# Kernel optimization log

Hardware: AMD Instinct MI355X
Metric: run time of the kernel (lower is better)

The kernel has to match this reference:

```python
import jax, jax.numpy as jnp
import numpy as np


def _square_distance(src, dst):
    # src: [B,N,C], dst: [B,M,C] -> [B,N,M] squared euclidean distances
    # ||s-d||^2 = -2 s.d + ||s||^2 + ||d||^2
    d = -2.0 * jnp.einsum('bnc,bmc->bnm', src, dst)
    d = d + jnp.sum(src * src, axis=-1)[:, :, None]
    d = d + jnp.sum(dst * dst, axis=-1)[:, None, :]
    return d


def setup_inputs() -> dict:
    key = jax.random.key(0)
    k1, k2 = jax.random.split(key)
    B, N, M, C = 8, 4096, 4096, 3
    f = jax.random.normal(k1, (B, N, C), dtype=jnp.float32)
    f_ = jax.random.normal(k2, (B, M, C), dtype=jnp.float32)
    return {"f": f, "f_": f_}


def reference(f, f_):
    dis = _square_distance(f, f_)          # [B,N,M]
    f2f_ = jnp.min(dis, axis=2)            # [B,N] nearest in f_ for each f point
    f_2f = jnp.min(dis, axis=1)            # [B,M] nearest in f for each f_ point
    d = jnp.mean(f2f_, axis=1) + jnp.mean(f_2f, axis=1)  # [B]
    return jnp.mean(d)
```

## Files before the change

### kernel.cpp

```cpp
#include <hip/hip_runtime.h>


typedef float v2f __attribute__((ext_vector_type(2)));

constexpr int B = 8;
constexpr int N = 4096;
constexpr int M = 4096;
constexpr int S = 16;
constexpr int TM = M / S;
constexpr int GPS = TM / 2;
constexpr int BLOCK = 256;
constexpr int Q = 8;
constexpr int QPB = BLOCK * Q;
constexpr int QCH = N / QPB;

__device__ __forceinline__ v2f pk_fma(v2f a, v2f b, v2f c) {
    v2f d;
    asm("v_pk_fma_f32 %0, %1, %2, %3" : "=v"(d) : "v"(a), "v"(b), "v"(c));
    return d;
}

__global__ __launch_bounds__(256, 2) void chamfer_dir_kernel(
    const float* __restrict__ f,
    const float* __restrict__ f_,
    unsigned int* __restrict__ minA,
    unsigned int* __restrict__ minB)
{
    __shared__ float4 sT[2 * GPS];

    const int dir = blockIdx.z;
    const int b   = blockIdx.y;
    const int seg = blockIdx.x & (S - 1);
    const int qc  = blockIdx.x >> 4;

    const float* qsrc = dir ? f_ : f;
    const float* tsrc = dir ? f  : f_;
    unsigned int* omin = dir ? minB : minA;

    {
        const int t = threadIdx.x;
        const float* tb = tsrc + ((size_t)b * M + (size_t)seg * TM + t) * 3;
        const float x = tb[0], y = tb[1], z = tb[2];
        const int g = t >> 1, h = t & 1;
        float* base = (float*)sT;
        base[8 * g + 0 + h] = -2.0f * x;
        base[8 * g + 2 + h] = -2.0f * y;
        base[8 * g + 4 + h] = -2.0f * z;
        base[8 * g + 6 + h] = x * x + y * y + z * z;
    }

    const int qbase = qc * QPB + threadIdx.x;
    const float* qb = qsrc + (size_t)b * N * 3;
    v2f qxv[Q], qyv[Q], qzv[Q];
    float qn[Q];
    #pragma unroll
    for (int j = 0; j < Q; ++j) {
        const int q = qbase + j * BLOCK;
        const float x = qb[3 * q + 0], y = qb[3 * q + 1], z = qb[3 * q + 2];
        qxv[j] = (v2f){x, x};
        qyv[j] = (v2f){y, y};
        qzv[j] = (v2f){z, z};
        qn[j] = x * x + y * y + z * z;
    }
    __syncthreads();

    float m[Q];
    #pragma unroll
    for (int j = 0; j < Q; ++j) m[j] = 3.402823466e+38f;

    #pragma unroll 2
    for (int g = 0; g < GPS; ++g) {
        const float4 r0 = sT[2 * g];
        const float4 r1 = sT[2 * g + 1];
        const v2f x01 = {r0.x, r0.y};
        const v2f y01 = {r0.z, r0.w};
        const v2f z01 = {r1.x, r1.y};
        const v2f w01 = {r1.z, r1.w};

        #pragma unroll
        for (int j = 0; j < Q; ++j) {
            v2f a = pk_fma(qzv[j], z01, w01);
            a = pk_fma(qyv[j], y01, a);
            a = pk_fma(qxv[j], x01, a);
            m[j] = fminf(fminf(m[j], a.x), a.y);
        }
    }

    #pragma unroll
    for (int j = 0; j < Q; ++j) {
        const float d = m[j] + qn[j];
        atomicMin(&omin[b * N + qbase + j * BLOCK], __float_as_uint(d));
    }
}

__global__ __launch_bounds__(256) void reduce_out_kernel(
    const uint4* __restrict__ mins,
    float* __restrict__ out)
{
    __shared__ float wsum[4];
    const int tid = threadIdx.x;
    const uint4 v = mins[blockIdx.x * 256 + tid];
    float s = (__uint_as_float(v.x) + __uint_as_float(v.y))
            + (__uint_as_float(v.z) + __uint_as_float(v.w));

    #pragma unroll
    for (int off = 32; off > 0; off >>= 1) s += __shfl_down(s, off, 64);
    if ((tid & 63) == 0) wsum[tid >> 6] = s;
    __syncthreads();
    if (tid == 0) {
        const float r = (wsum[0] + wsum[1]) + (wsum[2] + wsum[3]);
        atomicAdd(out, r * (1.0f / 32768.0f));
    }
}

extern "C" void kernel_launch(void* const* d_in, const int* in_sizes, int n_in,
                              void* d_out, int out_size, void* d_ws, size_t ws_size,
                              hipStream_t stream) {
    (void)in_sizes; (void)n_in; (void)out_size; (void)ws_size;
    const float* f  = (const float*)d_in[0];
    const float* f_ = (const float*)d_in[1];
    float* out = (float*)d_out;

    unsigned int* minA = (unsigned int*)d_ws;
    unsigned int* minB = minA + (size_t)B * N;

    dim3 grid(QCH * S, B, 2);
    chamfer_dir_kernel<<<grid, BLOCK, 0, stream>>>(f, f_, minA, minB);

    reduce_out_kernel<<<64, 256, 0, stream>>>((const uint4*)minA, out);
}
```

Measured before the change: 77.33 us.

## Compute both chamfer directions in one pass with split-bf16 MFMA tiles

```diff
diff --git a/kernel.cpp b/kernel.cpp
--- a/kernel.cpp
+++ b/kernel.cpp
@@ -1,96 +1,147 @@
 #include <hip/hip_runtime.h>
 
 
-typedef float v2f __attribute__((ext_vector_type(2)));
+typedef __attribute__((ext_vector_type(8))) short bf16x8;
+typedef __attribute__((ext_vector_type(4))) float f32x4;
 
 constexpr int B = 8;
 constexpr int N = 4096;
 constexpr int M = 4096;
-constexpr int S = 16;
-constexpr int TM = M / S;
-constexpr int GPS = TM / 2;
-constexpr int BLOCK = 256;
-constexpr int Q = 8;
-constexpr int QPB = BLOCK * Q;
-constexpr int QCH = N / QPB;
 
-__device__ __forceinline__ v2f pk_fma(v2f a, v2f b, v2f c) {
-    v2f d;
-    asm("v_pk_fma_f32 %0, %1, %2, %3" : "=v"(d) : "v"(a), "v"(b), "v"(c));
-    return d;
+constexpr int ROWS_PER_BLOCK = 128;
+constexpr int COL_CHUNK = 2048;
+constexpr int SEG = 512;
+constexpr int SEGS = COL_CHUNK / SEG;
+constexpr int CTILES = SEG / 16;
+
+static __device__ __forceinline__ unsigned short f2bf(float v) {
+    unsigned u = __float_as_uint(v);
+    return (unsigned short)((u + 0x7FFFu + ((u >> 16) & 1u)) >> 16);
+}
+static __device__ __forceinline__ float bf2f(unsigned short b) {
+    return __uint_as_float(((unsigned)b) << 16);
+}
+static __device__ __forceinline__ void split3(float v, unsigned short& a,
+                                              unsigned short& b, unsigned short& c) {
+    a = f2bf(v); float r = v - bf2f(a);
+    b = f2bf(r); r -= bf2f(b);
+    c = f2bf(r);
 }
 
-__global__ __launch_bounds__(256, 2) void chamfer_dir_kernel(
+__global__ __launch_bounds__(256, 2) void chamfer_mfma_kernel(
     const float* __restrict__ f,
     const float* __restrict__ f_,
     unsigned int* __restrict__ minA,
     unsigned int* __restrict__ minB)
 {
-    __shared__ float4 sT[2 * GPS];
+    __shared__ unsigned short Bv[SEG][32];
+    __shared__ unsigned int cmin[COL_CHUNK];
 
-    const int dir = blockIdx.z;
-    const int b   = blockIdx.y;
-    const int seg = blockIdx.x & (S - 1);
-    const int qc  = blockIdx.x >> 4;
+    const int tid  = threadIdx.x;
+    const int lane = tid & 63;
+    const int w    = tid >> 6;
+    const int r    = lane & 15;
+    const int kg   = lane >> 4;
 
-    const float* qsrc = dir ? f_ : f;
-    const float* tsrc = dir ? f  : f_;
-    unsigned int* omin = dir ? minB : minA;
+    const int b  = blockIdx.y;
+    const int rc = blockIdx.x >> 1;
+    const int cc = blockIdx.x & 1;
 
-    {
-        const int t = threadIdx.x;
-        const float* tb = tsrc + ((size_t)b * M + (size_t)seg * TM + t) * 3;
-        const float x = tb[0], y = tb[1], z = tb[2];
-        const int g = t >> 1, h = t & 1;
-        float* base = (float*)sT;
-        base[8 * g + 0 + h] = -2.0f * x;
-        base[8 * g + 2 + h] = -2.0f * y;
-        base[8 * g + 4 + h] = -2.0f * z;
-        base[8 * g + 6 + h] = x * x + y * y + z * z;
+    for (int i = tid; i < COL_CHUNK; i += 256) cmin[i] = 0xFFFFFFFFu;
+
+    const int rowbase = rc * ROWS_PER_BLOCK + w * 32;
+    bf16x8 a0, a1;
+    #pragma unroll
+    for (int rt = 0; rt < 2; ++rt) {
+        const float* qp = f + ((size_t)b * N + rowbase + rt * 16 + r) * 3;
+        const float x = qp[0], y = qp[1], z = qp[2];
+        unsigned short px0,px1,px2, py0,py1,py2, pz0,pz1,pz2, n0,n1,n2;
+        split3(-2.f * x, px0, px1, px2);
+        split3(-2.f * y, py0, py1, py2);
+        split3(-2.f * z, pz0, pz1, pz2);
+        split3(x*x + y*y + z*z, n0, n1, n2);
+        const short ONE = 0x3F80;
+        bf16x8 a;
+        if (kg == 0)
+            a = (bf16x8){(short)px0,(short)px0,(short)px1,(short)px1,(short)px0,(short)px2,(short)py0,(short)py0};
+        else if (kg == 1)
+            a = (bf16x8){(short)py1,(short)py1,(short)py0,(short)py2,(short)pz0,(short)pz0,(short)pz1,(short)pz1};
+        else if (kg == 2)
+            a = (bf16x8){(short)pz0,(short)pz2,(short)n0,(short)n1,(short)n2,ONE,ONE,ONE};
+        else
+            a = (bf16x8){0,0,0,0,0,0,0,0};
+        if (rt == 0) a0 = a; else a1 = a;
     }
 
-    const int qbase = qc * QPB + threadIdx.x;
-    const float* qb = qsrc + (size_t)b * N * 3;
-    v2f qxv[Q], qyv[Q], qzv[Q];
-    float qn[Q];
+    float rm0[4], rm1[4];
     #pragma unroll
-    for (int j = 0; j < Q; ++j) {
-        const int q = qbase + j * BLOCK;
-        const float x = qb[3 * q + 0], y = qb[3 * q + 1], z = qb[3 * q + 2];
-        qxv[j] = (v2f){x, x};
-        qyv[j] = (v2f){y, y};
-        qzv[j] = (v2f){z, z};
-        qn[j] = x * x + y * y + z * z;
-    }
-    __syncthreads();
+    for (int j = 0; j < 4; ++j) { rm0[j] = 3.402823466e+38f; rm1[j] = 3.402823466e+38f; }
 
-    float m[Q];
-    #pragma unroll
-    for (int j = 0; j < Q; ++j) m[j] = 3.402823466e+38f;
+    const float* tbase = f_ + ((size_t)b * M + (size_t)cc * COL_CHUNK) * 3;
+    const bf16x8* bunits = reinterpret_cast<const bf16x8*>(&Bv[0][0]);
+    const f32x4 zero = {0.f, 0.f, 0.f, 0.f};
 
-    #pragma unroll 2
-    for (int g = 0; g < GPS; ++g) {
-        const float4 r0 = sT[2 * g];
-        const float4 r1 = sT[2 * g + 1];
-        const v2f x01 = {r0.x, r0.y};
-        const v2f y01 = {r0.z, r0.w};
-        const v2f z01 = {r1.x, r1.y};
-        const v2f w01 = {r1.z, r1.w};
+    for (int s = 0; s < SEGS; ++s) {
+        __syncthreads();
+        #pragma unroll
+        for (int h = 0; h < 2; ++h) {
+            const int t = h * 256 + tid;
+            const float* tp = tbase + (size_t)(s * SEG + t) * 3;
+            const float x = tp[0], y = tp[1], z = tp[2];
+            unsigned short x0,x1,x2, y0,y1,y2, z0,z1,z2, m0,m1,m2;
+            split3(x, x0, x1, x2);
+            split3(y, y0, y1, y2);
+            split3(z, z0, z1, z2);
+            split3(x*x + y*y + z*z, m0, m1, m2);
+            const short ONE = 0x3F80;
+            bf16x8* dst = reinterpret_cast<bf16x8*>(&Bv[t][0]);
+            dst[0] = (bf16x8){(short)x0,(short)x1,(short)x0,(short)x1,(short)x2,(short)x0,(short)y0,(short)y1};
+            dst[1] = (bf16x8){(short)y0,(short)y1,(short)y2,(short)y0,(short)z0,(short)z1,(short)z0,(short)z1};
+            dst[2] = (bf16x8){(short)z2,(short)z0,ONE,ONE,ONE,(short)m0,(short)m1,(short)m2};
+            dst[3] = (bf16x8){0,0,0,0,0,0,0,0};
+        }
+        __syncthreads();
 
-        #pragma unroll
-        for (int j = 0; j < Q; ++j) {
-            v2f a = pk_fma(qzv[j], z01, w01);
-            a = pk_fma(qyv[j], y01, a);
-            a = pk_fma(qxv[j], x01, a);
-            m[j] = fminf(fminf(m[j], a.x), a.y);
+        bf16x8 bb = bunits[r * 4 + kg];
+        #pragma unroll 4
+        for (int ct = 0; ct < CTILES; ++ct) {
+            const int nct = (ct + 1) & (CTILES - 1);
+            bf16x8 nb = bunits[r * 4 + kg + nct * 64];
+            f32x4 c0 = __builtin_amdgcn_mfma_f32_16x16x32_bf16(a0, bb, zero, 0, 0, 0);
+            f32x4 c1 = __builtin_amdgcn_mfma_f32_16x16x32_bf16(a1, bb, zero, 0, 0, 0);
+            #pragma unroll
+            for (int j = 0; j < 4; ++j) {
+                rm0[j] = fminf(rm0[j], c0[j]);
+                rm1[j] = fminf(rm1[j], c1[j]);
+            }
+            float v = fminf(fminf(fminf(c0[0], c0[1]), fminf(c0[2], c0[3])),
+                            fminf(fminf(c1[0], c1[1]), fminf(c1[2], c1[3])));
+            v = fminf(v, __shfl_xor(v, 16));
+            v = fminf(v, __shfl_xor(v, 32));
+            if (lane < 16)
+                atomicMin(&cmin[s * SEG + ct * 16 + lane], __float_as_uint(v));
+            bb = nb;
         }
     }
 
     #pragma unroll
-    for (int j = 0; j < Q; ++j) {
-        const float d = m[j] + qn[j];
-        atomicMin(&omin[b * N + qbase + j * BLOCK], __float_as_uint(d));
+    for (int rt = 0; rt < 2; ++rt) {
+        #pragma unroll
+        for (int j = 0; j < 4; ++j) {
+            float v = rt ? rm1[j] : rm0[j];
+            v = fminf(v, __shfl_xor(v, 1));
+            v = fminf(v, __shfl_xor(v, 2));
+            v = fminf(v, __shfl_xor(v, 4));
+            v = fminf(v, __shfl_xor(v, 8));
+            if (r == 0) {
+                const int row = rowbase + rt * 16 + kg * 4 + j;
+                atomicMin(&minA[b * N + row], __float_as_uint(v));
+            }
+        }
     }
+    __syncthreads();
+    for (int i = tid; i < COL_CHUNK; i += 256)
+        atomicMin(&minB[b * M + cc * COL_CHUNK + i], cmin[i]);
 }
 
 __global__ __launch_bounds__(256) void reduce_out_kernel(
@@ -124,8 +175,8 @@
     unsigned int* minA = (unsigned int*)d_ws;
     unsigned int* minB = minA + (size_t)B * N;
 
-    dim3 grid(QCH * S, B, 2);
-    chamfer_dir_kernel<<<grid, BLOCK, 0, stream>>>(f, f_, minA, minB);
+    dim3 grid(64, 8);
+    chamfer_mfma_kernel<<<grid, 256, 0, stream>>>(f, f_, minA, minB);
 
     reduce_out_kernel<<<64, 256, 0, stream>>>((const uint4*)minA, out);
 }
```

Result: slower. 87.22 us (+12.8%).
